# Kernel tuning notes

Measured on AMD Instinct MI355X. Metric: run time of the kernel, lower is better.

The kernel has to match this reference:

```python
import jax, jax.numpy as jnp
import numpy as np

B, T, D = 2, 2048, 1024
H, HKV, HD = 16, 4, 64  # num_heads, num_kv_heads, head_dim
EPS = 1.1920929e-07  # torch.finfo(float32).eps, nn.RMSNorm default


def _rmsnorm(x, g):
    return x * jax.lax.rsqrt(jnp.mean(x * x, axis=-1, keepdims=True) + EPS) * g


def _ternary(w):
    # ternary quantize {-1,0,+1} with straight-through estimator
    th = jnp.mean(jnp.abs(w))
    wt = jnp.sign(w) * (jnp.abs(w) > th).astype(w.dtype)
    return w + jax.lax.stop_gradient(wt - w)


def _bitlinear(x, w, g):
    return _rmsnorm(x, g) @ _ternary(w).T


def setup_inputs() -> dict:
    key = jax.random.key(0)
    ks = jax.random.split(key, 5)
    kaiming = lambda k, shape: jax.random.normal(k, shape, jnp.float32) * np.float32(np.sqrt(2.0 / shape[1]))
    return {
        "x": jax.random.normal(ks[0], (B, T, D), jnp.float32),
        "q_w": kaiming(ks[1], (D, D)),
        "q_g": jnp.ones((D,), jnp.float32),
        "k_w": kaiming(ks[2], (HKV * HD, D)),
        "k_g": jnp.ones((D,), jnp.float32),
        "v_w": kaiming(ks[3], (HKV * HD, D)),
        "o_w": kaiming(ks[4], (D, D)),
        "o_g": jnp.ones((D,), jnp.float32),
        "qk_gain": jnp.float32(5.25),
    }


def reference(x, q_w, q_g, k_w, k_g, v_w, o_w, o_g, qk_gain):
    b, t, d = x.shape
    q = _bitlinear(x, q_w, q_g).reshape(b, t, H, HD)          # [B,T,H,hd]
    k = _bitlinear(x, k_w, k_g).reshape(b, t, HKV, HD)        # [B,T,Hkv,hd]
    v = (x @ v_w.T).reshape(b, t, HKV, HD)                    # [B,T,Hkv,hd]
    rep = H // HKV
    k = jnp.repeat(k, rep, axis=2)                            # GQA expand -> [B,T,H,hd]
    v = jnp.repeat(v, rep, axis=2)
    scale = qk_gain / np.float32(np.sqrt(HD))
    attn = jnp.einsum('bqhd,bkhd->bhqk', q, k) * scale        # [B,H,T,T]
    causal = jnp.tril(jnp.ones((t, t), bool))
    attn = jnp.where(causal, attn, -jnp.inf)
    attn = jax.nn.softmax(attn, axis=-1)
    out = jnp.einsum('bhqk,bkhd->bqhd', attn, v).reshape(b, t, d)
    return _bitlinear(out, o_w, o_g)
```

## Files before the change

### kernel.cpp

```cpp
#include <hip/hip_runtime.h>
#include <hip/hip_bf16.h>
#include <cstdint>
#include <cstddef>

typedef unsigned short u16;
typedef unsigned int u32;
typedef __attribute__((ext_vector_type(8))) short short8v;
typedef __attribute__((ext_vector_type(4))) float f32x4;
typedef __attribute__((ext_vector_type(4))) u16 u16x4;
typedef __attribute__((ext_vector_type(8))) u16 u16x8;

static constexpr int Bc = 2, Tc = 2048, Dc = 1024, Hc = 16, HKVc = 4, HDc = 64;
static constexpr int Mc = Bc * Tc;
static constexpr float EPSc = 1.1920929e-07f;

static __device__ __forceinline__ u16 f2bf(float f) {
  u32 u = __builtin_bit_cast(u32, f);
  return (u16)((u + 0x7fffu + ((u >> 16) & 1u)) >> 16);
}
static __device__ __forceinline__ float bf2f(u16 b) {
  u32 u = ((u32)b) << 16;
  return __builtin_bit_cast(float, u);
}
static __device__ __forceinline__ float fast_exp2(float x) {
  float r;
  asm("v_exp_f32 %0, %1" : "=v"(r) : "v"(x));
  return r;
}
static __device__ __forceinline__ u32 cvt_pk_bf16(float lo, float hi) {
  u32 r;
  asm("v_cvt_pk_bf16_f32 %0, %1, %2" : "=v"(r) : "v"(lo), "v"(hi));
  return r;
}

__global__ __launch_bounds__(256) void np_leafsum_all(const float* __restrict__ q_w,
                                                      const float* __restrict__ k_w,
                                                      const float* __restrict__ o_w,
                                                      float* __restrict__ leaf) {
  int blk = blockIdx.x;
  const float* w;
  float* out;
  int lfbase;
  if (blk < 256)      { w = q_w; out = leaf;         lfbase = blk * 32; }
  else if (blk < 320) { w = k_w; out = leaf + 8192;  lfbase = (blk - 256) * 32; }
  else                { w = o_w; out = leaf + 10240; lfbase = (blk - 320) * 32; }
  int t = threadIdx.x;
  int lf = lfbase + (t >> 3), j = t & 7;
  const float* a = w + (size_t)lf * 128;
  float r = fabsf(a[j]);
#pragma unroll
  for (int i = 8; i < 128; i += 8) r += fabsf(a[i + j]);
  float x = r + __shfl_xor(r, 1);
  float y = x + __shfl_xor(x, 2);
  float z = y + __shfl_xor(y, 4);
  if (j == 0) out[lf] = z;
}

__global__ __launch_bounds__(256) void np_treemean3(const float* __restrict__ leaf,
                                                    float* __restrict__ th) {
  int m = blockIdx.x;
  const float* src = leaf + (m == 0 ? 0 : (m == 1 ? 8192 : 10240));
  int nle = (m == 1) ? 2048 : 8192;
  float inv_n = (m == 1) ? (1.0f / 262144.0f) : (1.0f / 1048576.0f);
  int t = threadIdx.x;
  int chunk = nle >> 8;
  float v[32];
  for (int i = 0; i < chunk; i += 4) {
    float4 f = *(const float4*)&src[t * chunk + i];
    v[i] = f.x; v[i + 1] = f.y; v[i + 2] = f.z; v[i + 3] = f.w;
  }
  for (int cnt = chunk >> 1; cnt >= 1; cnt >>= 1)
    for (int i = 0; i < cnt; ++i) v[i] = v[2 * i] + v[2 * i + 1];
  float s = v[0];
#pragma unroll
  for (int off = 1; off < 64; off <<= 1) s += __shfl_xor(s, off);
  __shared__ float red[4];
  if ((t & 63) == 0) red[t >> 6] = s;
  __syncthreads();
  if (t == 0) th[m] = ((red[0] + red[1]) + (red[2] + red[3])) * inv_n;
}

__global__ __launch_bounds__(256) void quant_split_all(const float* __restrict__ q_w,
                                                       const float* __restrict__ k_w,
                                                       const float* __restrict__ o_w,
                                                       const float* __restrict__ v_w,
                                                       const float* __restrict__ th,
                                                       u16* __restrict__ Wq,
                                                       u16* __restrict__ Wk,
                                                       u16* __restrict__ Wo,
                                                       u16* __restrict__ Vwh) {
  int i4 = blockIdx.x * 256 + threadIdx.x;
  if (i4 < 589824) {
    const float* w; u16* o; float t;
    int j;
    if (i4 < 262144)      { w = q_w; o = Wq; t = th[0]; j = i4; }
    else if (i4 < 327680) { w = k_w; o = Wk; t = th[1]; j = i4 - 262144; }
    else                  { w = o_w; o = Wo; t = th[2]; j = i4 - 327680; }
    float4 v = *(const float4*)&w[(size_t)j * 4];
    float y[4] = {v.x, v.y, v.z, v.w};
    u16x4 q;
#pragma unroll
    for (int c = 0; c < 4; ++c)
      q[c] = (y[c] > t) ? (u16)0x3F80 : ((y[c] < -t) ? (u16)0xBF80 : (u16)0);
    *(u16x4*)&o[(size_t)j * 4] = q;
  } else {
    int j = i4 - 589824;
    float4 v = *(const float4*)&v_w[(size_t)j * 4];
    float y[4] = {v.x, v.y, v.z, v.w};
    u16x4 h;
#pragma unroll
    for (int c = 0; c < 4; ++c) h[c] = f2bf(y[c]);
    *(u16x4*)&Vwh[(size_t)j * 4] = h;
  }
}

__global__ __launch_bounds__(256) void rmsnorm_split6(const float* __restrict__ X,
                                                      const float* __restrict__ g1,
                                                      const float* __restrict__ g2,
                                                      u16* __restrict__ H1, u16* __restrict__ L1,
                                                      u16* __restrict__ H2, u16* __restrict__ L2,
                                                      u16* __restrict__ HV) {
  int row = blockIdx.x;
  const float* xr = X + (size_t)row * Dc;
  int tid = threadIdx.x;
  float4 v = *(const float4*)&xr[tid * 4];
  float vv[4] = {v.x, v.y, v.z, v.w};
  if (HV != nullptr) {
    u16x4 h;
#pragma unroll
    for (int j = 0; j < 4; ++j) h[j] = f2bf(vv[j]);
    *(u16x4*)&HV[(size_t)row * Dc + tid * 4] = h;
  }
  float ss = v.x * v.x + v.y * v.y + v.z * v.z + v.w * v.w;
#pragma unroll
  for (int off = 1; off < 64; off <<= 1) ss += __shfl_xor(ss, off);
  __shared__ float red[4];
  if ((tid & 63) == 0) red[tid >> 6] = ss;
  __syncthreads();
  float tot = red[0] + red[1] + red[2] + red[3];
  float inv = 1.0f / sqrtf(tot * (1.0f / (float)Dc) + EPSc);
  {
    float4 a = *(const float4*)&g1[tid * 4];
    float ga[4] = {a.x, a.y, a.z, a.w};
    u16x4 h, l;
#pragma unroll
    for (int j = 0; j < 4; ++j) {
      float y = vv[j] * inv * ga[j];
      u16 hb = f2bf(y);
      h[j] = hb;
      l[j] = f2bf(y - bf2f(hb));
    }
    *(u16x4*)&H1[(size_t)row * Dc + tid * 4] = h;
    if (L1 != nullptr) *(u16x4*)&L1[(size_t)row * Dc + tid * 4] = l;
  }
  if (g2 != nullptr) {
    float4 a = *(const float4*)&g2[tid * 4];
    float ga[4] = {a.x, a.y, a.z, a.w};
    u16x4 h, l;
#pragma unroll
    for (int j = 0; j < 4; ++j) {
      float y = vv[j] * inv * ga[j];
      u16 hb = f2bf(y);
      h[j] = hb;
      l[j] = f2bf(y - bf2f(hb));
    }
    *(u16x4*)&H2[(size_t)row * Dc + tid * 4] = h;
    if (L2 != nullptr) *(u16x4*)&L2[(size_t)row * Dc + tid * 4] = l;
  }
}

template <bool PA, int MODE>
static __device__ __forceinline__ void gemm_body(
    const u16* __restrict__ Ah, const u16* __restrict__ Al,
    const u16* __restrict__ Bh,
    int N, int K, int bm, int bn,
    float* __restrict__ C, u16* __restrict__ O1, u16* __restrict__ O2,
    u16* smem) {
  constexpr int APT = 2, BPT = 4;
  u16* AhS = smem;
  u16* AlS = smem + 4096;
  u16* BhS = smem + 8192;
  int tid = threadIdx.x;
  int l = tid & 63, w = tid >> 6;
  int wm = (w >> 1) * 32, wn = (w & 1) * 64;
  u16x8 rAh[APT], rAl[PA ? APT : 1], rBh[BPT];
  f32x4 acc[2][4] = {};
#define LOADTILE(kb_)                                                               \
  {                                                                                 \
    _Pragma("unroll") for (int p = 0; p < APT; ++p) {                               \
      int idx = tid + p * 256;                                                      \
      int row = idx >> 3, cc = idx & 7;                                             \
      rAh[p] = *(const u16x8*)&Ah[(size_t)(bm + row) * K + (kb_) + cc * 8];         \
      if (PA) rAl[p] = *(const u16x8*)&Al[(size_t)(bm + row) * K + (kb_) + cc * 8]; \
    }                                                                               \
    _Pragma("unroll") for (int p = 0; p < BPT; ++p) {                               \
      int idx = tid + p * 256;                                                      \
      int row = idx >> 3, cc = idx & 7;                                             \
      rBh[p] = *(const u16x8*)&Bh[(size_t)(bn + row) * K + (kb_) + cc * 8];         \
    }                                                                               \
  }
  LOADTILE(0)
  for (int kb = 0; kb < K; kb += 64) {
    __syncthreads();
#pragma unroll
    for (int p = 0; p < APT; ++p) {
      int idx = tid + p * 256;
      int row = idx >> 3, cc = idx & 7;
      int off = row * 64 + ((cc * 8) ^ ((row & 7) << 3));
      *(u16x8*)&AhS[off] = rAh[p];
      if (PA) *(u16x8*)&AlS[off] = rAl[p];
    }
#pragma unroll
    for (int p = 0; p < BPT; ++p) {
      int idx = tid + p * 256;
      int row = idx >> 3, cc = idx & 7;
      int off = row * 64 + ((cc * 8) ^ ((row & 7) << 3));
      *(u16x8*)&BhS[off] = rBh[p];
    }
    if (kb + 64 < K) LOADTILE(kb + 64)
    __syncthreads();
    __builtin_amdgcn_s_setprio(1);
#pragma unroll
    for (int sl = 0; sl < 2; ++sl) {
      short8v fa[2], fal[2], fb[4];
      int kof = (l >> 4) * 8 + sl * 32;
#pragma unroll
      for (int m = 0; m < 2; ++m) {
        int row = wm + m * 16 + (l & 15);
        int off = row * 64 + (kof ^ ((row & 7) << 3));
        fa[m] = *(const short8v*)&AhS[off];
        if (PA) fal[m] = *(const short8v*)&AlS[off];
      }
#pragma unroll
      for (int n = 0; n < 4; ++n) {
        int row = wn + n * 16 + (l & 15);
        int off = row * 64 + (kof ^ ((row & 7) << 3));
        fb[n] = *(const short8v*)&BhS[off];
      }
#pragma unroll
      for (int m = 0; m < 2; ++m)
#pragma unroll
        for (int n = 0; n < 4; ++n) {
          acc[m][n] = __builtin_amdgcn_mfma_f32_16x16x32_bf16(fa[m], fb[n], acc[m][n], 0, 0, 0);
          if (PA)
            acc[m][n] = __builtin_amdgcn_mfma_f32_16x16x32_bf16(fal[m], fb[n], acc[m][n], 0, 0, 0);
        }
    }
    __builtin_amdgcn_s_setprio(0);
  }
#undef LOADTILE
#pragma unroll
  for (int m = 0; m < 2; ++m)
#pragma unroll
    for (int n = 0; n < 4; ++n)
#pragma unroll
      for (int r = 0; r < 4; ++r) {
        int grow = bm + wm + m * 16 + (l >> 4) * 4 + r;
        int gcol = bn + wn + n * 16 + (l & 15);
        float v = acc[m][n][r];
        if (MODE == 0) {
          C[(size_t)grow * N + gcol] = v;
        } else if (MODE == 1) {
          u16 hb = f2bf(v);
          O1[(size_t)grow * N + gcol] = hb;
          O2[(size_t)grow * N + gcol] = f2bf(v - bf2f(hb));
        } else {
          int k = gcol & 31;
          int gp = (gcol & ~31) | (((k >> 2) & 3) << 3) |
                   (((k >> 4) & 1) << 2) | (k & 3);
          O1[(size_t)grow * N + gp] = f2bf(v);
        }
      }
}

__global__ __launch_bounds__(256, 1) void qkv_mega(
    const u16* __restrict__ Xqh, const u16* __restrict__ Xql, const u16* __restrict__ Wq,
    const u16* __restrict__ Xkh, const u16* __restrict__ Xkl, const u16* __restrict__ Wk,
    const u16* __restrict__ Xvh, const u16* __restrict__ Vwh,
    u16* __restrict__ Qh, u16* __restrict__ Ql,
    u16* __restrict__ Kh, u16* __restrict__ Kl,
    u16* __restrict__ Vt) {
  __shared__ __align__(16) u16 SMEM[16384];
  int bx = blockIdx.x;
  if (bx < 512) {
    int bm = (bx >> 3) * 64, bn = (bx & 7) * 128;
    gemm_body<true, 1>(Xqh, Xql, Wq, 1024, 1024, bm, bn, nullptr, Qh, Ql, SMEM);
  } else if (bx < 640) {
    int t = bx - 512;
    int bm = (t >> 1) * 64, bn = (t & 1) * 128;
    gemm_body<true, 1>(Xkh, Xkl, Wk, 256, 1024, bm, bn, nullptr, Kh, Kl, SMEM);
  } else {
    int t = bx - 640;
    int bm = (t >> 5) * 64, bn = (t & 31) * 128;
    gemm_body<false, 3>(Vwh, nullptr, Xvh, 4096, 1024, bm, bn, nullptr, Vt, nullptr, SMEM);
  }
}

__global__ __launch_bounds__(256, 1) void o_gemm(
    const u16* __restrict__ Ah, const u16* __restrict__ Bh,
    float* __restrict__ C) {
  __shared__ __align__(16) u16 SMEM[16384];
  int bm = blockIdx.y * 64, bn = blockIdx.x * 128;
  gemm_body<false, 0>(Ah, nullptr, Bh, 1024, 1024, bm, bn, C, nullptr, nullptr, SMEM);
}

__global__ __launch_bounds__(256, 2) void attn_mfma9(
    const u16* __restrict__ Qh, const u16* __restrict__ Ql,
    const u16* __restrict__ Kh, const u16* __restrict__ Kl,
    const u16* __restrict__ Vt,
    const float* __restrict__ qk_gain,
    float* __restrict__ AO) {
  __shared__ __align__(16) u16 SM[24576];
  int tid = threadIdx.x;
  int w = tid >> 6, l = tid & 63;
  int h = blockIdx.x & 15, b = blockIdx.x >> 4;
  int by = blockIdx.y;
  int qt = (by < 8) ? (15 - by) : (by - 8);
  int q0 = qt * 128;
  int kvh = h >> 2;
  const float sc2 = qk_gain[0] * 0.125f * 1.44269504f;
  u16x8 pk[2], pl[2], pv[2];
#define AISSUE3(K0)                                                             \
  {                                                                             \
    _Pragma("unroll") for (int p = 0; p < 2; ++p) {                             \
      int idx = tid + p * 256;                                                  \
      int jj = idx >> 3, cc = idx & 7;                                          \
      size_t kb = ((size_t)(b * Tc + (K0) + jj)) * (HKVc * HDc) + kvh * 64 + cc * 8; \
      pk[p] = *(const u16x8*)&Kh[kb];                                           \
      pl[p] = *(const u16x8*)&Kl[kb];                                           \
      size_t vb = ((size_t)(kvh * 64 + jj)) * (size_t)Mc + b * Tc + (K0) + cc * 8; \
      pv[p] = *(const u16x8*)&Vt[vb];                                           \
    }                                                                           \
  }
#define WRITEBUF(BI)                                                            \
  {                                                                             \
    u16* bb = SM + (BI) * 12288;                                                \
    _Pragma("unroll") for (int p = 0; p < 2; ++p) {                             \
      int idx = tid + p * 256;                                                  \
      int jj = idx >> 3, cc = idx & 7;                                          \
      int sw = jj * 64 + ((cc * 8) ^ ((jj & 7) << 3));                          \
      *(u16x8*)&bb[sw] = pk[p];                                                 \
      *(u16x8*)&bb[4096 + sw] = pl[p];                                          \
      *(u16x8*)&bb[8192 + sw] = pv[p];                                          \
    }                                                                           \
  }
  short8v qb_h[4], qb_l[4];
#pragma unroll
  for (int qp = 0; qp < 2; ++qp) {
    size_t qrow = (size_t)(b * Tc + q0 + w * 32 + qp * 16 + (l & 15));
#pragma unroll
    for (int sl = 0; sl < 2; ++sl) {
      int dstart = (l >> 4) * 8 + sl * 32;
      qb_h[qp * 2 + sl] = *(const short8v*)&Qh[qrow * Dc + h * 64 + dstart];
      qb_l[qp * 2 + sl] = *(const short8v*)&Ql[qrow * Dc + h * 64 + dstart];
    }
  }
  f32x4 Oacc[8] = {{0,0,0,0},{0,0,0,0},{0,0,0,0},{0,0,0,0},
                   {0,0,0,0},{0,0,0,0},{0,0,0,0},{0,0,0,0}};
  float mrow[2] = {-3.0e38f, -3.0e38f};
  float lrow[2] = {0.f, 0.f};
  int qmax_w = q0 + w * 32 + 31;
  int nsteps = 2 * qt + 2;
  AISSUE3(0)
  WRITEBUF(0)
  AISSUE3(64)
  __syncthreads();
  for (int stp = 0; stp < nsteps; ++stp) {
    int k0 = stp * 64;
    u16* Kh_s = SM + (stp & 1) * 12288;
    u16* Kl_s = Kh_s + 4096;
    u16* Vt_s = Kh_s + 8192;
    if (stp + 1 < nsteps) WRITEBUF((stp + 1) & 1)
    if (stp + 2 < nsteps) AISSUE3((stp + 2) * 64)
    if (k0 <= qmax_w) {
      f32x4 s[8] = {{0,0,0,0},{0,0,0,0},{0,0,0,0},{0,0,0,0},
                    {0,0,0,0},{0,0,0,0},{0,0,0,0},{0,0,0,0}};
      __builtin_amdgcn_s_setprio(1);
#pragma unroll
      for (int kt = 0; kt < 4; ++kt) {
        int key = kt * 16 + (l & 15);
#pragma unroll
        for (int sl = 0; sl < 2; ++sl) {
          int dstart = ((l >> 4) * 8 + 32 * sl) ^ ((key & 7) << 3);
          short8v bh = *(const short8v*)&Kh_s[key * 64 + dstart];
          short8v bl = *(const short8v*)&Kl_s[key * 64 + dstart];
#pragma unroll
          for (int qp = 0; qp < 2; ++qp) {
            s[qp * 4 + kt] = __builtin_amdgcn_mfma_f32_16x16x32_bf16(bh, qb_h[qp * 2 + sl], s[qp * 4 + kt], 0, 0, 0);
            s[qp * 4 + kt] = __builtin_amdgcn_mfma_f32_16x16x32_bf16(bl, qb_h[qp * 2 + sl], s[qp * 4 + kt], 0, 0, 0);
            s[qp * 4 + kt] = __builtin_amdgcn_mfma_f32_16x16x32_bf16(bh, qb_l[qp * 2 + sl], s[qp * 4 + kt], 0, 0, 0);
          }
        }
      }
      __builtin_amdgcn_s_setprio(0);
      bool full = (k0 + 63) <= (q0 + w * 32);
      if (!full) {
#pragma unroll
        for (int qp = 0; qp < 2; ++qp) {
          int qg = q0 + w * 32 + qp * 16 + (l & 15);
#pragma unroll
          for (int kt = 0; kt < 4; ++kt)
#pragma unroll
            for (int r = 0; r < 4; ++r)
              if (k0 + kt * 16 + ((l >> 4) << 2) + r > qg) s[qp * 4 + kt][r] = -3.0e38f;
        }
      }
      float p[2][4][4];
#pragma unroll
      for (int qp = 0; qp < 2; ++qp) {
        float mk[4];
#pragma unroll
        for (int kt = 0; kt < 4; ++kt)
          mk[kt] = fmaxf(fmaxf(s[qp * 4 + kt][0], s[qp * 4 + kt][1]),
                         fmaxf(s[qp * 4 + kt][2], s[qp * 4 + kt][3]));
        float mx = fmaxf(fmaxf(mk[0], mk[1]), fmaxf(mk[2], mk[3]));
        mx = fmaxf(mx, __shfl_xor(mx, 16));
        mx = fmaxf(mx, __shfl_xor(mx, 32));
        float mnew = fmaxf(mrow[qp], mx);
        float msc = mnew * sc2;
        float corr = fast_exp2(__builtin_fmaf(mrow[qp], sc2, -msc));
        mrow[qp] = mnew;
        float sk[4];
#pragma unroll
        for (int kt = 0; kt < 4; ++kt) {
#pragma unroll
          for (int r = 0; r < 4; ++r)
            p[qp][kt][r] = fast_exp2(__builtin_fmaf(s[qp * 4 + kt][r], sc2, -msc));
          sk[kt] = (p[qp][kt][0] + p[qp][kt][1]) + (p[qp][kt][2] + p[qp][kt][3]);
        }
        float rs = (sk[0] + sk[1]) + (sk[2] + sk[3]);
        rs += __shfl_xor(rs, 16);
        rs += __shfl_xor(rs, 32);
        lrow[qp] = lrow[qp] * corr + rs;
#pragma unroll
        for (int dt = 0; dt < 4; ++dt) Oacc[qp * 4 + dt] *= corr;
      }
      short8v fbv[4];
#pragma unroll
      for (int qp = 0; qp < 2; ++qp)
#pragma unroll
        for (int sl = 0; sl < 2; ++sl) {
          union { u32 u[4]; short8v v; } fq;
          fq.u[0] = cvt_pk_bf16(p[qp][2 * sl][0], p[qp][2 * sl][1]);
          fq.u[1] = cvt_pk_bf16(p[qp][2 * sl][2], p[qp][2 * sl][3]);
          fq.u[2] = cvt_pk_bf16(p[qp][2 * sl + 1][0], p[qp][2 * sl + 1][1]);
          fq.u[3] = cvt_pk_bf16(p[qp][2 * sl + 1][2], p[qp][2 * sl + 1][3]);
          fbv[qp * 2 + sl] = fq.v;
        }
      __builtin_amdgcn_s_setprio(1);
#pragma unroll
      for (int dt = 0; dt < 4; ++dt) {
        int d = dt * 16 + (l & 15);
#pragma unroll
        for (int sl = 0; sl < 2; ++sl) {
          int kstart = ((l >> 4) * 8 + 32 * sl) ^ ((d & 7) << 3);
          short8v fav = *(const short8v*)&Vt_s[d * 64 + kstart];
#pragma unroll
          for (int qp = 0; qp < 2; ++qp)
            Oacc[qp * 4 + dt] = __builtin_amdgcn_mfma_f32_16x16x32_bf16(fav, fbv[qp * 2 + sl], Oacc[qp * 4 + dt], 0, 0, 0);
        }
      }
      __builtin_amdgcn_s_setprio(0);
    }
    __syncthreads();
  }
  float* Es = (float*)SM + w * (16 * 68);
#pragma unroll
  for (int qp = 0; qp < 2; ++qp) {
    float invl = 1.0f / lrow[qp];
#pragma unroll
    for (int dt = 0; dt < 4; ++dt)
#pragma unroll
      for (int r = 0; r < 4; ++r)
        Es[(l & 15) * 68 + dt * 16 + ((l >> 4) << 2) + r] = Oacc[qp * 4 + dt][r] * invl;
    size_t arow = ((size_t)(b * Tc + q0 + w * 32 + qp * 16 + (l >> 2))) * Dc + h * 64 + (l & 3) * 4;
#pragma unroll
    for (int j = 0; j < 4; ++j) {
      float4 vv = *(const float4*)&Es[(l >> 2) * 68 + (l & 3) * 4 + j * 16];
      *(float4*)&AO[arow + j * 16] = vv;
    }
  }
#undef AISSUE3
#undef WRITEBUF
}

extern "C" void kernel_launch(void* const* d_in, const int* in_sizes, int n_in,
                              void* d_out, int out_size, void* d_ws, size_t ws_size,
                              hipStream_t stream) {
  const float* x    = (const float*)d_in[0];
  const float* q_w  = (const float*)d_in[1];
  const float* q_g  = (const float*)d_in[2];
  const float* k_w  = (const float*)d_in[3];
  const float* k_g  = (const float*)d_in[4];
  const float* v_w  = (const float*)d_in[5];
  const float* o_w  = (const float*)d_in[6];
  const float* o_g  = (const float*)d_in[7];
  const float* qk_g = (const float*)d_in[8];

  char* base = (char*)d_ws;
  u16* Xqh = (u16*)(base + (0ull  << 20));
  u16* Xql = (u16*)(base + (8ull  << 20));
  u16* Xkh = (u16*)(base + (16ull << 20));
  u16* Xkl = (u16*)(base + (24ull << 20));
  u16* Xvh = (u16*)(base + (32ull << 20));
  u16* Qh  = (u16*)(base + (40ull << 20));
  u16* Ql  = (u16*)(base + (48ull << 20));
  u16* Kh  = (u16*)(base + (56ull << 20));
  u16* Kl  = (u16*)(base + (58ull << 20));
  u16* Vt  = (u16*)(base + (60ull << 20));
  u16* Wq  = (u16*)(base + (62ull << 20));
  u16* Wk  = (u16*)(base + (64ull << 20));
  u16* Wo  = (u16*)(base + (64ull << 20) + (512ull << 10));
  u16* Vwh = (u16*)(base + (66ull << 20) + (512ull << 10));
  float* leaf = (float*)(base + (67ull << 20));
  float* th   = leaf + 18432;
  float* AO  = (float*)base;
  u16* Xoh = Xkh;

  np_leafsum_all<<<576, 256, 0, stream>>>(q_w, k_w, o_w, leaf);
  np_treemean3<<<3, 256, 0, stream>>>(leaf, th);

  quant_split_all<<<2560, 256, 0, stream>>>(q_w, k_w, o_w, v_w, th, Wq, Wk, Wo, Vwh);

  rmsnorm_split6<<<Mc, 256, 0, stream>>>(x, q_g, k_g, Xqh, Xql, Xkh, Xkl, Xvh);

  qkv_mega<<<768, 256, 0, stream>>>(Xqh, Xql, Wq, Xkh, Xkl, Wk, Xvh, Vwh,
                                    Qh, Ql, Kh, Kl, Vt);

  attn_mfma9<<<dim3(32, 16, 1), 256, 0, stream>>>(Qh, Ql, Kh, Kl, Vt, qk_g, AO);

  rmsnorm_split6<<<Mc, 256, 0, stream>>>(AO, o_g, nullptr, Xoh, nullptr, nullptr, nullptr,
                                         nullptr);
  o_gemm<<<dim3(8, 64), 256, 0, stream>>>(Xoh, Wo, (float*)d_out);
}
```

Baseline: 138.7 us.

## Split causal attention over KV chunks with a separate merge kernel

Splits the causal flash-attention over KV ranges of up to 8 steps per block, giving 40 work items per head instead of 16 query tiles of very uneven length. Each partial writes an unnormalized bf16 output plus per-row max and sum, and a new merge kernel combines the partials with log-sum-exp rescaling into the fp32 AO buffer. Occupancy is raised to 3 blocks per CU. The aim is better load balance and fuller use of the GPU, paid for with an extra kernel launch, extra partial-output traffic, and bf16 rounding of the partial outputs.

```diff
diff --git a/kernel.cpp b/kernel.cpp
--- a/kernel.cpp
+++ b/kernel.cpp
@@ -304,20 +304,28 @@
   gemm_body<false, 0>(Ah, nullptr, Bh, 1024, 1024, bm, bn, C, nullptr, nullptr, SMEM);
 }
 
-__global__ __launch_bounds__(256, 2) void attn_mfma9(
+__global__ __launch_bounds__(256, 3) void attn_part(
     const u16* __restrict__ Qh, const u16* __restrict__ Ql,
     const u16* __restrict__ Kh, const u16* __restrict__ Kl,
     const u16* __restrict__ Vt,
     const float* __restrict__ qk_gain,
-    float* __restrict__ AO) {
+    u16* __restrict__ Opart, float* __restrict__ MLpart) {
   __shared__ __align__(16) u16 SM[24576];
   int tid = threadIdx.x;
   int w = tid >> 6, l = tid & 63;
-  int h = blockIdx.x & 15, b = blockIdx.x >> 4;
-  int by = blockIdx.y;
-  int qt = (by < 8) ? (15 - by) : (by - 8);
+  int hb = blockIdx.x;
+  int h = hb & 15, b = hb >> 4;
+  int kvh = h >> 2;
+  int f = blockIdx.y;
+  int qt, ci;
+  if (f < 4)       { qt = f; ci = 0; }
+  else if (f < 12) { int o = f - 4;  qt = 4 + (o >> 1); ci = o & 1; }
+  else if (f < 24) { int o = f - 12; qt = 8 + o / 3;    ci = o - (o / 3) * 3; }
+  else             { int o = f - 24; qt = 12 + (o >> 2); ci = o & 3; }
   int q0 = qt * 128;
-  int kvh = h >> 2;
+  int tsteps = 2 * qt + 2;
+  int s0 = ci * 8;
+  int s1 = (s0 + 8 < tsteps) ? (s0 + 8) : tsteps;
   const float sc2 = qk_gain[0] * 0.125f * 1.44269504f;
   u16x8 pk[2], pl[2], pv[2];
 #define AISSUE3(K0)                                                             \
@@ -360,18 +368,18 @@
   float mrow[2] = {-3.0e38f, -3.0e38f};
   float lrow[2] = {0.f, 0.f};
   int qmax_w = q0 + w * 32 + 31;
-  int nsteps = 2 * qt + 2;
-  AISSUE3(0)
+  AISSUE3(s0 * 64)
   WRITEBUF(0)
-  AISSUE3(64)
+  if (s0 + 1 < s1) AISSUE3((s0 + 1) * 64)
   __syncthreads();
-  for (int stp = 0; stp < nsteps; ++stp) {
+  for (int li = 0; li < s1 - s0; ++li) {
+    int stp = s0 + li;
     int k0 = stp * 64;
-    u16* Kh_s = SM + (stp & 1) * 12288;
+    u16* Kh_s = SM + (li & 1) * 12288;
     u16* Kl_s = Kh_s + 4096;
     u16* Vt_s = Kh_s + 8192;
-    if (stp + 1 < nsteps) WRITEBUF((stp + 1) & 1)
-    if (stp + 2 < nsteps) AISSUE3((stp + 2) * 64)
+    if (stp + 1 < s1) WRITEBUF((li + 1) & 1)
+    if (stp + 2 < s1) AISSUE3((stp + 2) * 64)
     if (k0 <= qmax_w) {
       f32x4 s[8] = {{0,0,0,0},{0,0,0,0},{0,0,0,0},{0,0,0,0},
                     {0,0,0,0},{0,0,0,0},{0,0,0,0},{0,0,0,0}};
@@ -464,24 +472,79 @@
     }
     __syncthreads();
   }
-  float* Es = (float*)SM + w * (16 * 68);
+  int G = hb * 40 + f;
+  u16* Op = Opart + (size_t)G * 8192;
+  float* Es = (float*)SM + w * 1088;
 #pragma unroll
   for (int qp = 0; qp < 2; ++qp) {
-    float invl = 1.0f / lrow[qp];
 #pragma unroll
     for (int dt = 0; dt < 4; ++dt)
 #pragma unroll
       for (int r = 0; r < 4; ++r)
-        Es[(l & 15) * 68 + dt * 16 + ((l >> 4) << 2) + r] = Oacc[qp * 4 + dt][r] * invl;
-    size_t arow = ((size_t)(b * Tc + q0 + w * 32 + qp * 16 + (l >> 2))) * Dc + h * 64 + (l & 3) * 4;
+        Es[(l & 15) * 68 + dt * 16 + ((l >> 4) << 2) + r] = Oacc[qp * 4 + dt][r];
+    int qloc = w * 32 + qp * 16 + (l >> 2);
 #pragma unroll
     for (int j = 0; j < 4; ++j) {
       float4 vv = *(const float4*)&Es[(l >> 2) * 68 + (l & 3) * 4 + j * 16];
-      *(float4*)&AO[arow + j * 16] = vv;
+      u16x4 o4;
+      o4[0] = f2bf(vv.x); o4[1] = f2bf(vv.y); o4[2] = f2bf(vv.z); o4[3] = f2bf(vv.w);
+      *(u16x4*)&Op[qloc * 64 + (l & 3) * 4 + j * 16] = o4;
+    }
+  }
+  if (l < 16) {
+#pragma unroll
+    for (int qp = 0; qp < 2; ++qp) {
+      int qloc = w * 32 + qp * 16 + l;
+      MLpart[(size_t)G * 256 + qloc * 2 + 0] = mrow[qp];
+      MLpart[(size_t)G * 256 + qloc * 2 + 1] = lrow[qp];
     }
   }
 #undef AISSUE3
 #undef WRITEBUF
+}
+
+__global__ __launch_bounds__(256) void attn_merge(const u16* __restrict__ Opart,
+                                                  const float* __restrict__ MLpart,
+                                                  const float* __restrict__ qk_gain,
+                                                  float* __restrict__ AO) {
+  int hb = blockIdx.x;
+  int h = hb & 15, b = hb >> 4;
+  int qt = blockIdx.y;
+  int g = qt >> 2, rr = qt & 3;
+  int cum = 2 * g * (g + 1) + rr * (g + 1);
+  int nc = (2 * qt + 9) >> 3;
+  const float sc2 = qk_gain[0] * 0.125f * 1.44269504f;
+  int t = threadIdx.x;
+  int q = t >> 1, dh = (t & 1) * 32;
+  size_t Gbase = (size_t)hb * 40 + cum;
+  float mi[4], li[4];
+  float M = -3.0e38f;
+  for (int i = 0; i < nc; ++i) {
+    mi[i] = MLpart[(Gbase + i) * 256 + q * 2 + 0];
+    li[i] = MLpart[(Gbase + i) * 256 + q * 2 + 1];
+    M = fmaxf(M, mi[i]);
+  }
+  float acc[32] = {};
+  float L = 0.0f;
+  for (int i = 0; i < nc; ++i) {
+    float wgt = fast_exp2((mi[i] - M) * sc2);
+    L += wgt * li[i];
+    const u16* Op = Opart + (Gbase + i) * 8192 + q * 64 + dh;
+#pragma unroll
+    for (int c = 0; c < 4; ++c) {
+      u16x8 v8 = *(const u16x8*)&Op[c * 8];
+#pragma unroll
+      for (int j = 0; j < 8; ++j) acc[c * 8 + j] += wgt * bf2f(v8[j]);
+    }
+  }
+  float inv = 1.0f / L;
+  size_t arow = ((size_t)(b * Tc + qt * 128 + q)) * Dc + h * 64 + dh;
+#pragma unroll
+  for (int c = 0; c < 8; ++c) {
+    float4 o = make_float4(acc[c * 4] * inv, acc[c * 4 + 1] * inv,
+                           acc[c * 4 + 2] * inv, acc[c * 4 + 3] * inv);
+    *(float4*)&AO[arow + c * 4] = o;
+  }
 }
 
 extern "C" void kernel_launch(void* const* d_in, const int* in_sizes, int n_in,
@@ -514,8 +577,10 @@
   u16* Vwh = (u16*)(base + (66ull << 20) + (512ull << 10));
   float* leaf = (float*)(base + (67ull << 20));
   float* th   = leaf + 18432;
-  float* AO  = (float*)base;
-  u16* Xoh = Xkh;
+  float* AO     = (float*)base;
+  u16*  Opart   = (u16*)(base + (16ull << 20));
+  float* MLpart = (float*)(base + (36ull << 20));
+  u16*  Xoh     = (u16*)(base + (16ull << 20));
 
   np_leafsum_all<<<576, 256, 0, stream>>>(q_w, k_w, o_w, leaf);
   np_treemean3<<<3, 256, 0, stream>>>(leaf, th);
@@ -527,7 +592,8 @@
   qkv_mega<<<768, 256, 0, stream>>>(Xqh, Xql, Wq, Xkh, Xkl, Wk, Xvh, Vwh,
                                     Qh, Ql, Kh, Kl, Vt);
 
-  attn_mfma9<<<dim3(32, 16, 1), 256, 0, stream>>>(Qh, Ql, Kh, Kl, Vt, qk_g, AO);
+  attn_part<<<dim3(32, 40), 256, 0, stream>>>(Qh, Ql, Kh, Kl, Vt, qk_g, Opart, MLpart);
+  attn_merge<<<dim3(32, 16), 256, 0, stream>>>(Opart, MLpart, qk_g, AO);
 
   rmsnorm_split6<<<Mc, 256, 0, stream>>>(AO, o_g, nullptr, Xoh, nullptr, nullptr, nullptr,
                                          nullptr);
```

Result: no change. 141.4 us (+2.0%).
